# Optimization experiments

Measured on AMD Instinct MI355X. Metric: run time of the kernel, lower is better.

Reference implementation:

```python
import jax, jax.numpy as jnp
import numpy as np

# Model dims (match init_kwargs)
D_MODEL = 1024
EXP = 2
D_IN = D_MODEL * EXP      # 2048, channels after input projection
D_STATE = 16
CONV_D = 4
BATCH = 4
SEQ = 2048


def setup_inputs() -> dict:
    key = jax.random.key(0)
    ks = jax.random.split(key, 8)
    sd = 1.0 / np.sqrt(D_MODEL)
    sdi = 1.0 / np.sqrt(D_IN)
    return {
        "x": jax.random.normal(ks[0], (BATCH, SEQ, D_MODEL), jnp.float32),
        "norm_w": jnp.ones((D_MODEL,), jnp.float32),
        "Win": jax.random.normal(ks[1], (D_MODEL, D_IN), jnp.float32) * sd,
        "b_in": jnp.zeros((D_IN,), jnp.float32),
        # depthwise conv kernel: [out=D_IN, in/groups=1, K]
        "conv_w": jax.random.normal(ks[2], (D_IN, 1, CONV_D), jnp.float32) * 0.5,
        "conv_b": jnp.zeros((D_IN,), jnp.float32),
        # A scaled by 0.1 so per-channel 16x16 transition has spectral radius < 1
        # (torch.randn A would overflow over 2048 recurrence steps)
        "A": jax.random.normal(ks[3], (D_IN, D_STATE, D_STATE), jnp.float32) * 0.1,
        "Bm": jax.random.normal(ks[4], (D_IN, D_STATE, 1), jnp.float32),
        "Cm": jax.random.normal(ks[5], (D_IN, 1, D_STATE), jnp.float32),
        "Wout": jax.random.normal(ks[6], (D_IN, D_MODEL), jnp.float32) * sdi,
        "b_out": jnp.zeros((D_MODEL,), jnp.float32),
    }


def _rmsnorm(x, w, eps=1e-6):
    return x * jax.lax.rsqrt(jnp.mean(x * x, axis=-1, keepdims=True) + eps) * w


def reference(x, norm_w, Win, b_in, conv_w, conv_b, A, Bm, Cm, Wout, b_out):
    res = x
    h = _rmsnorm(x, norm_w)
    u = h @ Win + b_in                         # [B,L,D]
    u = u.transpose(0, 2, 1)                   # [B,D,L]
    # causal depthwise conv: pad (K-1,K-1) then slice [:L] == left-pad (K-1,0)
    u = jax.lax.conv_general_dilated(
        u, conv_w, window_strides=(1,), padding=[(CONV_D - 1, 0)],
        feature_group_count=D_IN,
        dimension_numbers=("NCH", "OIH", "NCH")) + conv_b[None, :, None]
    u = u.transpose(0, 2, 1)                   # [B,L,D]

    Bv = Bm[:, :, 0]                           # [D,S]
    Cv = Cm[:, 0, :]                           # [D,S]

    def step(hc, u_t):                         # hc [B,D,S], u_t [B,D]
        hc = jnp.einsum("bdr,drs->bds", hc, A) + u_t[:, :, None] * Bv[None]
        y = jnp.einsum("bds,ds->bd", hc, Cv)
        return hc, y

    h0 = jnp.zeros((x.shape[0], D_IN, D_STATE), u.dtype)
    _, ys = jax.lax.scan(step, h0, u.transpose(1, 0, 2))  # ys [L,B,D]
    y = ys.transpose(1, 0, 2)                  # [B,L,D]
    return y @ Wout + b_out + res
```

## Files before the change

### kernel.cpp

```cpp
#include <hip/hip_runtime.h>
#include <cstddef>

#define D_MODEL 1024
#define D_IN    2048
#define D_STATE 16
#define BATCH   4
#define SEQ     2048
#define NROWS   (BATCH * SEQ)
#define LTAPS   16
#define ETAPS   20
#define CH_BLK  32
#define T_BLK   128
#define U0LOG   152
#define NCH8    19
#define U0S     192
#define TPSS    20

typedef __attribute__((ext_vector_type(8))) short bf16x8;
typedef __attribute__((ext_vector_type(4))) float f32x4;
typedef unsigned short u16;


__device__ __forceinline__ void split_bf16(float f, short& hi, short& lo) {
    unsigned int u = __float_as_uint(f);
    hi = (short)(u >> 16);
    float fhi = __uint_as_float(u & 0xFFFF0000u);
    lo = (short)(__float_as_uint(f - fhi) >> 16);
}

__device__ __forceinline__ short rne_bf16(float f) {
    unsigned int u = __float_as_uint(f);
    return (short)((u + 0x7FFFu + ((u >> 16) & 1u)) >> 16);
}

__device__ __forceinline__ void gload16(const void* g, void* l) {
    __builtin_amdgcn_global_load_lds(
        (const __attribute__((address_space(1))) unsigned int*)g,
        (__attribute__((address_space(3))) unsigned int*)l, 16, 0, 0);
}

template<int CTRL>
__device__ __forceinline__ float dpp_mov(float v) {
    return __uint_as_float((unsigned)__builtin_amdgcn_update_dpp(
        0, (int)__float_as_uint(v), CTRL, 0xF, 0xF, false));
}

__device__ __forceinline__ int u0phys(int r, int ch) {
    return ch ^ (((ch >> 3) ^ r ^ (r >> 3)) & 7);
}

__global__ void rmsnorm_kernel(const float* __restrict__ x,
                               const float* __restrict__ w,
                               u16* __restrict__ hh) {
    const int row = blockIdx.x;
    const int c = threadIdx.x;
    const float* xr = x + (size_t)row * D_MODEL;

    float4 va = reinterpret_cast<const float4*>(xr)[c * 2 + 0];
    float4 vb = reinterpret_cast<const float4*>(xr)[c * 2 + 1];
    float ss = va.x*va.x + va.y*va.y + va.z*va.z + va.w*va.w
             + vb.x*vb.x + vb.y*vb.y + vb.z*vb.z + vb.w*vb.w;
    #pragma unroll
    for (int off = 32; off > 0; off >>= 1) ss += __shfl_down(ss, off, 64);

    __shared__ float ws2[2];
    if ((threadIdx.x & 63) == 0) ws2[threadIdx.x >> 6] = ss;
    __syncthreads();
    const float tot = ws2[0] + ws2[1];
    const float scale = rsqrtf(tot * (1.0f / D_MODEL) + 1e-6f);

    float4 wa = reinterpret_cast<const float4*>(w)[c * 2 + 0];
    float4 wb = reinterpret_cast<const float4*>(w)[c * 2 + 1];
    float o[8] = { va.x*scale*wa.x, va.y*scale*wa.y, va.z*scale*wa.z, va.w*scale*wa.w,
                   vb.x*scale*wb.x, vb.y*scale*wb.y, vb.z*scale*wb.z, vb.w*scale*wb.w };
    bf16x8 vh;
    #pragma unroll
    for (int e = 0; e < 8; ++e) vh[e] = rne_bf16(o[e]);

    const size_t eb = (size_t)row * D_MODEL + (size_t)(c & ~7) * 8
                    + (size_t)((c & 7) ^ (row & 7)) * 8;
    *reinterpret_cast<bf16x8*>(&hh[eb]) = vh;
}

__global__ void transpose_cast_kernel(const float* __restrict__ in,
                                      u16* __restrict__ oh,
                                      int R, int C) {
    __shared__ float T[64][65];
    const int r0 = blockIdx.y * 64, c0 = blockIdx.x * 64;
    const int t = threadIdx.x;

    #pragma unroll
    for (int i = 0; i < 4; ++i) {
        const int r = (t >> 4) + i * 16;
        float4 v = *reinterpret_cast<const float4*>(
            &in[(size_t)(r0 + r) * C + c0 + (t & 15) * 4]);
        T[r][(t & 15) * 4 + 0] = v.x;
        T[r][(t & 15) * 4 + 1] = v.y;
        T[r][(t & 15) * 4 + 2] = v.z;
        T[r][(t & 15) * 4 + 3] = v.w;
    }
    __syncthreads();

    #pragma unroll
    for (int g = 0; g < 2; ++g) {
        const int idx = t + g * 256;
        const int c  = idx >> 3;
        const int rg = idx & 7;
        bf16x8 vh;
        #pragma unroll
        for (int e = 0; e < 8; ++e) vh[e] = rne_bf16(T[rg * 8 + e][c]);
        const int orow = c0 + c;
        const size_t ob = (size_t)orow * R + r0 + (size_t)(rg ^ (orow & 7)) * 8;
        *reinterpret_cast<bf16x8*>(&oh[ob]) = vh;
    }
}

template<int KTOT, int EPI>
__global__ __launch_bounds__(512, 4) void gemm_gll(
    const u16* __restrict__ Ag, const u16* __restrict__ Bg,
    const float* __restrict__ bias, const float* __restrict__ resid,
    void* __restrict__ outp) {
    __shared__ __align__(16) char lds[65536];

    constexpr int GX  = (EPI == 0) ? (D_IN / 128) : (D_MODEL / 128);
    constexpr int NWG = GX * (NROWS / 128);
    const int orig = blockIdx.y * GX + blockIdx.x;
    const int swz  = (orig & 7) * (NWG >> 3) + (orig >> 3);
    const int sbx  = swz % GX;
    const int sby  = swz / GX;

    const int t = threadIdx.x;
    const int wv = t >> 6, lane = t & 63;
    const int lr = lane & 15, kb = lane >> 4;
    const int wr = (wv & 3) * 32;
    const int wc = (wv >> 2) * 64;
    const int a_r0 = (EPI == 0 ? sbx : sby) * 128;
    const int b_r0 = (EPI == 0 ? sby : sbx) * 128;

    const bool isA = (wv < 4);
    const int qrow = (wv & 3) * 32;
    const u16* garr = isA ? Ag : Bg;
    const int grow0 = (isA ? a_r0 : b_r0) + qrow;
    const int lboff = (isA ? 0 : 16384) + (qrow << 7);
    const u16* gsrc = garr + (size_t)(grow0 + (lane >> 3)) * KTOT + (lane & 7) * 8;

    f32x4 acc[2][4];
    #pragma unroll
    for (int i = 0; i < 2; ++i)
        #pragma unroll
        for (int j = 0; j < 4; ++j) acc[i][j] = (f32x4)(0.f);

    {
        char* lb = lds + lboff;
        #pragma unroll
        for (int sgi = 0; sgi < 4; ++sgi)
            gload16(gsrc + (size_t)sgi * 8 * KTOT, lb + sgi * 1024);
    }
    __syncthreads();

    int cur = 0;
    for (int k0 = 0; k0 < KTOT; k0 += 64) {
        if (k0 + 64 < KTOT) {
            const u16* gk = gsrc + k0 + 64;
            char* lb = lds + (cur ^ 1) * 32768 + lboff;
            #pragma unroll
            for (int sgi = 0; sgi < 4; ++sgi)
                gload16(gk + (size_t)sgi * 8 * KTOT, lb + sgi * 1024);
        }

        char* labase = lds + cur * 32768;
        char* lbbase = labase + 16384;
        #pragma unroll
        for (int ks = 0; ks < 2; ++ks) {
            bf16x8 afh[2], bfh[4];
            #pragma unroll
            for (int i = 0; i < 2; ++i) {
                const int ra = wr + i * 16 + lr;
                const int oa = (ra << 7) + (((ks * 4 + kb) ^ (ra & 7)) << 4);
                afh[i] = *reinterpret_cast<const bf16x8*>(labase + oa);
            }
            #pragma unroll
            for (int j = 0; j < 4; ++j) {
                const int rb = wc + j * 16 + lr;
                const int ob = (rb << 7) + (((ks * 4 + kb) ^ (rb & 7)) << 4);
                bfh[j] = *reinterpret_cast<const bf16x8*>(lbbase + ob);
            }
            #pragma unroll
            for (int i = 0; i < 2; ++i)
                #pragma unroll
                for (int j = 0; j < 4; ++j)
                    acc[i][j] = __builtin_amdgcn_mfma_f32_16x16x32_bf16(afh[i], bfh[j], acc[i][j], 0, 0, 0);
        }
        __syncthreads();
        cur ^= 1;
    }

    if (EPI == 0) {
        u16* up = (u16*)outp;
        const int b = b_r0 >> 11;
        const int s_base = b_r0 & (SEQ - 1);
        #pragma unroll
        for (int i = 0; i < 2; ++i) {
            #pragma unroll
            for (int r = 0; r < 4; ++r) {
                const int d = a_r0 + wr + i * 16 + kb * 4 + r;
                const float bb = bias[d];
                u16* dst = up + (size_t)b * D_IN * SEQ + (size_t)d * SEQ + s_base;
                #pragma unroll
                for (int j = 0; j < 4; ++j)
                    dst[wc + j * 16 + lr] = (u16)rne_bf16(acc[i][j][r] + bb);
            }
        }
    } else {
        float* op = (float*)outp;
        #pragma unroll
        for (int i = 0; i < 2; ++i) {
            #pragma unroll
            for (int r = 0; r < 4; ++r) {
                const int row = a_r0 + wr + i * 16 + kb * 4 + r;
                #pragma unroll
                for (int j = 0; j < 4; ++j) {
                    const int col = b_r0 + wc + j * 16 + lr;
                    op[(size_t)row * D_MODEL + col] =
                        acc[i][j][r] + bias[col] + resid[(size_t)row * D_MODEL + col];
                }
            }
        }
    }
}

__global__ __launch_bounds__(256) void prep_taps(
    const float* __restrict__ A, const float* __restrict__ Bm,
    const float* __restrict__ Cm,
    const float* __restrict__ conv_w, const float* __restrict__ conv_b,
    float* __restrict__ etaps, float* __restrict__ bt) {
    __shared__ float cS[16][33];
    const int wv = threadIdx.x >> 6;
    const int lane = threadIdx.x & 63;
    const int s = lane & 15;
    const int cl = wv * 4 + (lane >> 4);
    const int d0 = blockIdx.x * 16;
    const int d = d0 + cl;

    float a_col[16];
    #pragma unroll
    for (int r = 0; r < 16; ++r) a_col[r] = A[(size_t)d * 256 + r * 16 + s];
    float v = Bm[d * 16 + s];
    const float cv = Cm[d * 16 + s];

    for (int j = 0; j < LTAPS; ++j) {
        float t = v * cv;
        t += dpp_mov<0x118>(t);
        t += dpp_mov<0x114>(t);
        t += dpp_mov<0x112>(t);
        t += dpp_mov<0x111>(t);
        if (s == 15) cS[cl][j] = t;
        float n0 = 0.f, n1 = 0.f, n2 = 0.f, n3 = 0.f;
#define UP(r, nn) nn = fmaf(dpp_mov<0x150 + (r)>(v), a_col[r], nn);
        UP(0,n0) UP(1,n1) UP(2,n2) UP(3,n3)
        UP(4,n0) UP(5,n1) UP(6,n2) UP(7,n3)
        UP(8,n0) UP(9,n1) UP(10,n2) UP(11,n3)
        UP(12,n0) UP(13,n1) UP(14,n2) UP(15,n3)
#undef UP
        v = (n0 + n1) + (n2 + n3);
    }
    __syncthreads();

    for (int u = threadIdx.x; u < 16 * ETAPS; u += 256) {
        const int ch = u / ETAPS, m = u % ETAPS;
        float e = 0.f;
        #pragma unroll
        for (int dm = 0; dm < 4; ++dm) {
            const int j = m - dm;
            if (j >= 0 && j < LTAPS)
                e = fmaf(conv_w[(d0 + ch) * 4 + (3 - dm)], cS[ch][j], e);
        }
        etaps[(size_t)(d0 + ch) * ETAPS + m] = e;
    }
    for (int u = threadIdx.x; u < 16 * 64; u += 256) {
        const int ch = u >> 6, t = u & 63;
        float S = 0.f;
        for (int j = 0; j <= t && j < LTAPS; ++j) S += cS[ch][j];
        bt[(size_t)(d0 + ch) * 64 + t] = conv_b[d0 + ch] * S;
    }
}

__global__ __launch_bounds__(512, 6) void filter_scan(
    const u16* __restrict__ u0b,
    const float* __restrict__ etaps,
    const float* __restrict__ bt,
    u16* __restrict__ y2h) {
    __shared__ float U0[CH_BLK * U0S];
    __shared__ float TPS[CH_BLK * TPSS];

    const int tid = threadIdx.x;
    const int dg  = blockIdx.x;
    const int b   = blockIdx.y >> 4;
    const int t0  = (blockIdx.y & 15) << 7;
    const int d0  = dg * CH_BLK;

    #pragma unroll
    for (int k = 0; k < 2; ++k) {
        const int unit = tid + k * 512;
        if (unit < CH_BLK * NCH8) {
            const int cs = unit / NCH8;
            const int jc = unit % NCH8;
            const int gt = t0 - 24 + jc * 8;
            float v[8];
            if (gt >= 0) {
                bf16x8 bv = *reinterpret_cast<const bf16x8*>(
                    u0b + ((size_t)b * D_IN + d0 + cs) * SEQ + gt);
                #pragma unroll
                for (int e = 0; e < 8; ++e)
                    v[e] = __uint_as_float(((unsigned)(unsigned short)bv[e]) << 16);
            } else {
                #pragma unroll
                for (int e = 0; e < 8; ++e) v[e] = 0.f;
            }
            float4 lo = {v[0], v[1], v[2], v[3]};
            float4 hi = {v[4], v[5], v[6], v[7]};
            *reinterpret_cast<float4*>(&U0[cs * U0S + u0phys(cs, 2 * jc + 0) * 4]) = lo;
            *reinterpret_cast<float4*>(&U0[cs * U0S + u0phys(cs, 2 * jc + 1) * 4]) = hi;
        }
    }
    #pragma unroll
    for (int k = 0; k < 2; ++k) {
        const int unit = tid + k * 512;
        if (unit < CH_BLK * TPSS) {
            const int cs = unit / TPSS;
            const int m = unit % TPSS;
            TPS[cs * TPSS + m] = etaps[(size_t)(d0 + cs) * ETAPS + m];
        }
    }
    __syncthreads();

    const int c = tid >> 4;
    const int q = tid & 15;
    const int d = d0 + c;
    float* ucr = &U0[c * U0S];
    const float* tpr = &TPS[c * TPSS];

    #define LD4(ch) (*reinterpret_cast<const float4*>(&ucr[u0phys(c, (ch)) * 4]))

    float W[12];
    {
        float4 a  = LD4(2 * q + 5);
        float4 b4 = LD4(2 * q + 6);
        float4 c4 = LD4(2 * q + 7);
        W[0]=a.x; W[1]=a.y; W[2]=a.z; W[3]=a.w;
        W[4]=b4.x; W[5]=b4.y; W[6]=b4.z; W[7]=b4.w;
        W[8]=c4.x; W[9]=c4.y; W[10]=c4.z; W[11]=c4.w;
    }
    float acc[8];
    #pragma unroll
    for (int o = 0; o < 8; ++o) acc[o] = 0.f;

    #pragma unroll
    for (int jg = 0; jg < 5; ++jg) {
        const float4 ct = *reinterpret_cast<const float4*>(&tpr[jg * 4]);
        #pragma unroll
        for (int o = 0; o < 8; ++o) {
            acc[o] = fmaf(ct.x, W[o + 4], acc[o]);
            acc[o] = fmaf(ct.y, W[o + 3], acc[o]);
            acc[o] = fmaf(ct.z, W[o + 2], acc[o]);
            acc[o] = fmaf(ct.w, W[o + 1], acc[o]);
        }
        if (jg < 4) {
            #pragma unroll
            for (int m = 11; m >= 4; --m) W[m] = W[m - 4];
            const float4 nl = LD4(2 * q + 4 - jg);
            W[0]=nl.x; W[1]=nl.y; W[2]=nl.z; W[3]=nl.w;
        }
    }

    {
        const float cbS = bt[(size_t)d * 64 + 63];
        if (t0 == 0) {
            #pragma unroll
            for (int o = 0; o < 8; ++o) {
                const int tl = q * 8 + o;
                acc[o] += (tl >= 63) ? cbS : bt[(size_t)d * 64 + tl];
            }
        } else {
            #pragma unroll
            for (int o = 0; o < 8; ++o) acc[o] += cbS;
        }
    }

    __syncthreads();
    {
        float4 y0 = {acc[0], acc[1], acc[2], acc[3]};
        float4 y1 = {acc[4], acc[5], acc[6], acc[7]};
        *reinterpret_cast<float4*>(&ucr[u0phys(c, 2 * q + 0) * 4]) = y0;
        *reinterpret_cast<float4*>(&ucr[u0phys(c, 2 * q + 1) * 4]) = y1;
    }
    __syncthreads();
    #undef LD4

    const int lcb = (dg & 1) * 4;
    const int w64 = (dg >> 1) * 64;
    {
        const int t = tid >> 2;
        const int qc = tid & 3;
        const int tch = t >> 2, tof = t & 3;
        const size_t orow = (size_t)b * SEQ + t0 + t;
        const int phys = (lcb + qc) ^ (int)(orow & 7);
        int hv[4];
        #pragma unroll
        for (int k = 0; k < 4; ++k) {
            const int r0w = qc * 8 + 2 * k;
            const short h0 = rne_bf16(U0[(r0w + 0) * U0S + u0phys(r0w + 0, tch) * 4 + tof]);
            const short h1 = rne_bf16(U0[(r0w + 1) * U0S + u0phys(r0w + 1, tch) * 4 + tof]);
            hv[k] = (int)(unsigned short)h0 | ((int)(unsigned short)h1 << 16);
        }
        const size_t eb = orow * D_IN + w64 + (size_t)phys * 8;
        int4 hq = {hv[0], hv[1], hv[2], hv[3]};
        *reinterpret_cast<int4*>(&y2h[eb]) = hq;
    }
}

extern "C" void kernel_launch(void* const* d_in, const int* in_sizes, int n_in,
                              void* d_out, int out_size, void* d_ws, size_t ws_size,
                              hipStream_t stream) {
    const float* x      = (const float*)d_in[0];
    const float* norm_w = (const float*)d_in[1];
    const float* Win    = (const float*)d_in[2];
    const float* b_in   = (const float*)d_in[3];
    const float* conv_w = (const float*)d_in[4];
    const float* conv_b = (const float*)d_in[5];
    const float* A      = (const float*)d_in[6];
    const float* Bm     = (const float*)d_in[7];
    const float* Cm     = (const float*)d_in[8];
    const float* Wout   = (const float*)d_in[9];
    const float* b_out  = (const float*)d_in[10];
    float* out = (float*)d_out;

    char* W = (char*)d_ws;
    u16* u0b  = (u16*)W;
    u16* Wth  = (u16*)(W + ((size_t)64 << 20));
    u16* y2h  = (u16*)(W + ((size_t)64 << 20));
    u16* Woth = (u16*)W;
    u16* hh = (u16*)d_out;
    float* etaps = (float*)d_out;
    float* bt    = (float*)((char*)d_out + ((size_t)1 << 20));

    {
        dim3 g(D_IN / 64, D_MODEL / 64);
        transpose_cast_kernel<<<g, 256, 0, stream>>>(Win, Wth, D_MODEL, D_IN);
    }
    rmsnorm_kernel<<<NROWS, 128, 0, stream>>>(x, norm_w, hh);
    {
        dim3 grid(D_IN / 128, NROWS / 128);
        gemm_gll<D_MODEL, 0><<<grid, 512, 0, stream>>>(
            Wth, hh, b_in, nullptr, u0b);
    }
    prep_taps<<<D_IN / 16, 256, 0, stream>>>(A, Bm, Cm, conv_w, conv_b, etaps, bt);
    {
        dim3 g(D_IN / CH_BLK, BATCH * (SEQ / T_BLK));
        filter_scan<<<g, 512, 0, stream>>>(u0b, etaps, bt, y2h);
    }
    {
        dim3 g(D_MODEL / 64, D_IN / 64);
        transpose_cast_kernel<<<g, 256, 0, stream>>>(Wout, Woth, D_IN, D_MODEL);
    }
    {
        dim3 grid(D_MODEL / 128, NROWS / 128);
        gemm_gll<D_IN, 1><<<grid, 512, 0, stream>>>(
            y2h, Woth, b_out, x, out);
    }
}
```

Baseline: 123.1 us.

## Switch GEMM to 4-stage K=32 LDS pipeline with matching swizzled operand layouts

The bf16 GEMM main loop moves from a double-buffered K=64 tile to a four-buffer ring of K=32 tiles, with three loads in flight and explicit vmcnt waits plus raw s_barrier in place of __syncthreads. To keep the direct global-to-LDS copies conflict-free at the smaller tile width, the producer kernels (rmsnorm, transpose-cast, scan output) now write operands in a new 4-chunk rotation swizzle instead of the 8-chunk XOR swizzle. This aims to hide global load latency better and cut barrier stalls per k-step. The cost is more iterations and barriers overall, and correctness now depends on the hand-written wait counts and on all producers agreeing on the swizzle.

```diff
diff --git a/kernel.cpp b/kernel.cpp
--- a/kernel.cpp
+++ b/kernel.cpp
@@ -77,8 +77,8 @@
     #pragma unroll
     for (int e = 0; e < 8; ++e) vh[e] = rne_bf16(o[e]);
 
-    const size_t eb = (size_t)row * D_MODEL + (size_t)(c & ~7) * 8
-                    + (size_t)((c & 7) ^ (row & 7)) * 8;
+    const size_t eb = (size_t)row * D_MODEL + (size_t)(c & ~3) * 8
+                    + (size_t)(((c & 3) + (row >> 1)) & 3) * 8;
     *reinterpret_cast<bf16x8*>(&hh[eb]) = vh;
 }
 
@@ -110,7 +110,8 @@
         #pragma unroll
         for (int e = 0; e < 8; ++e) vh[e] = rne_bf16(T[rg * 8 + e][c]);
         const int orow = c0 + c;
-        const size_t ob = (size_t)orow * R + r0 + (size_t)(rg ^ (orow & 7)) * 8;
+        const size_t ob = (size_t)orow * R + r0 + (rg >> 2) * 32
+                        + (size_t)(((rg & 3) + (orow >> 1)) & 3) * 8;
         *reinterpret_cast<bf16x8*>(&oh[ob]) = vh;
     }
 }
@@ -124,6 +125,7 @@
 
     constexpr int GX  = (EPI == 0) ? (D_IN / 128) : (D_MODEL / 128);
     constexpr int NWG = GX * (NROWS / 128);
+    constexpr int NT  = KTOT / 32;
     const int orig = blockIdx.y * GX + blockIdx.x;
     const int swz  = (orig & 7) * (NWG >> 3) + (orig >> 3);
     const int sbx  = swz % GX;
@@ -141,8 +143,8 @@
     const int qrow = (wv & 3) * 32;
     const u16* garr = isA ? Ag : Bg;
     const int grow0 = (isA ? a_r0 : b_r0) + qrow;
-    const int lboff = (isA ? 0 : 16384) + (qrow << 7);
-    const u16* gsrc = garr + (size_t)(grow0 + (lane >> 3)) * KTOT + (lane & 7) * 8;
+    const int lboff = (isA ? 0 : 8192) + qrow * 64;
+    const u16* gsrc = garr + (size_t)(grow0 + (lane >> 2)) * KTOT + (lane & 3) * 8;
 
     f32x4 acc[2][4];
     #pragma unroll
@@ -150,50 +152,61 @@
         #pragma unroll
         for (int j = 0; j < 4; ++j) acc[i][j] = (f32x4)(0.f);
 
-    {
-        char* lb = lds + lboff;
-        #pragma unroll
-        for (int sgi = 0; sgi < 4; ++sgi)
-            gload16(gsrc + (size_t)sgi * 8 * KTOT, lb + sgi * 1024);
-    }
-    __syncthreads();
-
-    int cur = 0;
-    for (int k0 = 0; k0 < KTOT; k0 += 64) {
-        if (k0 + 64 < KTOT) {
-            const u16* gk = gsrc + k0 + 64;
-            char* lb = lds + (cur ^ 1) * 32768 + lboff;
-            #pragma unroll
-            for (int sgi = 0; sgi < 4; ++sgi)
-                gload16(gk + (size_t)sgi * 8 * KTOT, lb + sgi * 1024);
-        }
-
-        char* labase = lds + cur * 32768;
-        char* lbbase = labase + 16384;
-        #pragma unroll
-        for (int ks = 0; ks < 2; ++ks) {
-            bf16x8 afh[2], bfh[4];
-            #pragma unroll
-            for (int i = 0; i < 2; ++i) {
-                const int ra = wr + i * 16 + lr;
-                const int oa = (ra << 7) + (((ks * 4 + kb) ^ (ra & 7)) << 4);
-                afh[i] = *reinterpret_cast<const bf16x8*>(labase + oa);
-            }
-            #pragma unroll
-            for (int j = 0; j < 4; ++j) {
-                const int rb = wc + j * 16 + lr;
-                const int ob = (rb << 7) + (((ks * 4 + kb) ^ (rb & 7)) << 4);
-                bfh[j] = *reinterpret_cast<const bf16x8*>(lbbase + ob);
-            }
-            #pragma unroll
-            for (int i = 0; i < 2; ++i)
-                #pragma unroll
-                for (int j = 0; j < 4; ++j)
-                    acc[i][j] = __builtin_amdgcn_mfma_f32_16x16x32_bf16(afh[i], bfh[j], acc[i][j], 0, 0, 0);
-        }
-        __syncthreads();
-        cur ^= 1;
-    }
+#define STAGE(kt_) { \
+        const u16* gk = gsrc + (size_t)(kt_) * 32; \
+        char* lb = lds + ((kt_) & 3) * 16384 + lboff; \
+        gload16(gk, lb); \
+        gload16(gk + (size_t)16 * KTOT, lb + 1024); \
+    }
+#define COMPUTE(kt_) { \
+        char* labase = lds + ((kt_) & 3) * 16384; \
+        char* lbbase = labase + 8192; \
+        bf16x8 afh[2], bfh[4]; \
+        _Pragma("unroll") \
+        for (int i = 0; i < 2; ++i) { \
+            const int ra = wr + i * 16 + lr; \
+            const int oa = (ra << 6) + (((kb + (ra >> 1)) & 3) << 4); \
+            afh[i] = *reinterpret_cast<const bf16x8*>(labase + oa); \
+        } \
+        _Pragma("unroll") \
+        for (int j = 0; j < 4; ++j) { \
+            const int rb = wc + j * 16 + lr; \
+            const int ob = (rb << 6) + (((kb + (rb >> 1)) & 3) << 4); \
+            bfh[j] = *reinterpret_cast<const bf16x8*>(lbbase + ob); \
+        } \
+        _Pragma("unroll") \
+        for (int i = 0; i < 2; ++i) \
+            _Pragma("unroll") \
+            for (int j = 0; j < 4; ++j) \
+                acc[i][j] = __builtin_amdgcn_mfma_f32_16x16x32_bf16(afh[i], bfh[j], acc[i][j], 0, 0, 0); \
+    }
+
+    STAGE(0) STAGE(1) STAGE(2)
+    asm volatile("s_waitcnt vmcnt(4)" ::: "memory");
+    __builtin_amdgcn_s_barrier();
+    __builtin_amdgcn_sched_barrier(0);
+
+    int kt = 0;
+    for (; kt < NT - 3; ++kt) {
+        STAGE(kt + 3)
+        COMPUTE(kt)
+        asm volatile("s_waitcnt vmcnt(4)" ::: "memory");
+        __builtin_amdgcn_s_barrier();
+        __builtin_amdgcn_sched_barrier(0);
+    }
+    COMPUTE(kt)
+    asm volatile("s_waitcnt vmcnt(2)" ::: "memory");
+    __builtin_amdgcn_s_barrier();
+    __builtin_amdgcn_sched_barrier(0);
+    ++kt;
+    COMPUTE(kt)
+    asm volatile("s_waitcnt vmcnt(0)" ::: "memory");
+    __builtin_amdgcn_s_barrier();
+    __builtin_amdgcn_sched_barrier(0);
+    ++kt;
+    COMPUTE(kt)
+#undef STAGE
+#undef COMPUTE
 
     if (EPI == 0) {
         u16* up = (u16*)outp;
@@ -397,14 +410,12 @@
     __syncthreads();
     #undef LD4
 
-    const int lcb = (dg & 1) * 4;
-    const int w64 = (dg >> 1) * 64;
     {
         const int t = tid >> 2;
         const int qc = tid & 3;
         const int tch = t >> 2, tof = t & 3;
         const size_t orow = (size_t)b * SEQ + t0 + t;
-        const int phys = (lcb + qc) ^ (int)(orow & 7);
+        const int phys = (qc + (int)((orow >> 1) & 3)) & 3;
         int hv[4];
         #pragma unroll
         for (int k = 0; k < 4; ++k) {
@@ -413,7 +424,7 @@
             const short h1 = rne_bf16(U0[(r0w + 1) * U0S + u0phys(r0w + 1, tch) * 4 + tof]);
             hv[k] = (int)(unsigned short)h0 | ((int)(unsigned short)h1 << 16);
         }
-        const size_t eb = orow * D_IN + w64 + (size_t)phys * 8;
+        const size_t eb = orow * D_IN + (size_t)dg * 32 + (size_t)phys * 8;
         int4 hq = {hv[0], hv[1], hv[2], hv[3]};
         *reinterpret_cast<int4*>(&y2h[eb]) = hq;
     }
```

Result: slower. 136.5 us (+10.9%).
